# Performance work log

Measured on AMD Instinct MI355X. Metric: run time of the kernel, lower is better.

Reference implementation:

```python
import jax, jax.numpy as jnp
import numpy as np

GC_LAMBDA = 0.5   # smoothness weight from __init__
N_SWEEPS = 30     # fixed checkerboard ICM sweeps (each sweep = 2 half-updates)
EPS = 1e-6


def setup_inputs() -> dict:
    key = jax.random.key(0)
    probs = jax.random.uniform(key, (1, 4096, 4096), dtype=jnp.float32)
    return {"probs": probs}


def _nbr_sum(x):
    # sum of 4-connected neighbors with zero padding at the border
    p = jnp.pad(x, 1)
    return p[:-2, 1:-1] + p[2:, 1:-1] + p[1:-1, :-2] + p[1:-1, 2:]


def reference(probs) -> jnp.ndarray:
    """Graph-cut style binarization of a probability map.

    Minimizes the Potts energy
        E(y) = sum_i [ -y_i log p_i - (1-y_i) log(1-p_i) ]
               + lambda * sum_{(i,j) in 4-nbrs} [y_i != y_j]
    The original custom op solves this exactly via min-cut/max-flow; here we
    use the standard fully-vectorized checkerboard ICM relaxation of the same
    energy (fixed number of sweeps, jit-friendly, deterministic).
    """
    p = probs[0]                                   # [H, W]
    u1 = -jnp.log(p + EPS)                         # unary cost of label 1
    u0 = -jnp.log1p(-(p - EPS))                    # unary cost of label 0
    H, W = p.shape
    ncnt = _nbr_sum(jnp.ones((H, W), p.dtype))     # neighbor counts (2/3/4)
    ii = jnp.arange(H)[:, None]
    jj = jnp.arange(W)[None, :]
    parity_map = ((ii + jj) % 2).astype(jnp.int32)  # checkerboard coloring

    labels0 = (p > 0.5).astype(p.dtype)            # init from thresholding

    def half_sweep(labels, parity):
        ns = _nbr_sum(labels)                      # neighbors labeled 1
        cost1 = u1 + GC_LAMBDA * (ncnt - ns)       # disagree with 0-neighbors
        cost0 = u0 + GC_LAMBDA * ns                # disagree with 1-neighbors
        new = (cost1 < cost0).astype(labels.dtype)
        upd = parity_map == parity
        return jnp.where(upd, new, labels), None

    parities = jnp.tile(jnp.array([0, 1], jnp.int32), N_SWEEPS)
    labels, _ = jax.lax.scan(half_sweep, labels0, parities)
    return jnp.expand_dims(labels, axis=0)         # [1, H, W]
```

## Files before the change

kernel.cpp:

```cpp
#include <hip/hip_runtime.h>
#include <math.h>

#define HH 4096
#define WW 4096
#define WPR 64
#define NWORDS (HH * WPR)
typedef unsigned long long u64;

#define TILE_R 128
#define HALO_R 60
#define REG_R  248
#define REG_WC 10
#define RWORDS (REG_R * REG_WC)
#define NTHR   1024
#define WPT    3
#define NSWEEP 60
#define PACK_WPW 16

__device__ __forceinline__ bool decision(float p, int ncnt, int ns) {
    double pd = (double)p;
    double u1 = -log(pd + 1e-6);
    double u0 = -log1p(-(pd - 1e-6));
    double cost1 = u1 + 0.5 * (double)(ncnt - ns);
    double cost0 = u0 + 0.5 * (double)ns;
    return cost1 < cost0;
}

__global__ void setup_kernel(float* __restrict__ C) {
    int t = threadIdx.x;
    if (t >= 15) return;
    int ncnt = 2 + t / 5;
    int ns = t % 5;
    double T = 0.5 * (double)(2 * ns - ncnt);
    double eT = exp(T);
    double p0 = (1.0 + 1e-6 - 1e-6 * eT) / (1.0 + eT);
    float f0 = (float)p0;
    if (f0 < 0.0f) f0 = 0.0f;
    if (f0 > 1.0f) f0 = 1.0f;
    unsigned b0 = __float_as_uint(f0);
    unsigned lo = (b0 > 64u) ? b0 - 64u : 0u;
    unsigned hi = (b0 + 64u < 0x3F800000u) ? b0 + 64u : 0x3F800000u;
    if (decision(__uint_as_float(lo), ncnt, ns)) lo = 0u;
    if (!decision(__uint_as_float(hi), ncnt, ns)) hi = 0x3F800000u;
    while (hi - lo > 1u) {
        unsigned mid = lo + (hi - lo) / 2u;
        if (decision(__uint_as_float(mid), ncnt, ns)) hi = mid; else lo = mid;
    }
    C[t] = __uint_as_float(hi);
}

__global__ __launch_bounds__(256)
void pack_kernel(const float* __restrict__ probs, const float* __restrict__ C,
                 u64* __restrict__ Kp) {
    int gwave = (blockIdx.x * 256 + threadIdx.x) >> 6;
    int lane = threadIdx.x & 63;
    int w0 = gwave * PACK_WPW;
    float p[PACK_WPW];
#pragma unroll
    for (int q = 0; q < PACK_WPW; ++q)
        p[q] = probs[((size_t)(w0 + q) << 6) + lane];
    const float c0 = C[10], c1 = C[11], c2 = C[12], c3 = C[13], c4 = C[14];
#pragma unroll
    for (int q = 0; q < PACK_WPW; ++q) {
        int w = w0 + q;
        int i = w >> 6;
        int jbase = (w & 63) << 6;
        float pp = p[q];
        int k = (pp < c0) + (pp < c1) + (pp < c2) + (pp < c3) + (pp < c4);
        bool gE0 = (i == 0), gE1 = (i == HH - 1);
        bool jE0 = (jbase == 0) & (lane == 0);
        bool jE1 = (jbase == WW - 64) & (lane == 63);
        if (gE0 | gE1 | jE0 | jE1) {
            int ncnt = 4 - gE0 - gE1 - jE0 - jE1;
            const float* Cr = C + (ncnt - 2) * 5;
            k = (pp < Cr[0]) + (pp < Cr[1]) + (pp < Cr[2]) + (pp < Cr[3]) + (pp < Cr[4]);
        }
        u64 lb = __ballot(pp > 0.5f);
        u64 b0 = __ballot(k & 1);
        u64 b1 = __ballot(k & 2);
        u64 b2 = __ballot(k & 4);
        if (lane < 4) {
            u64 v = (lane == 0) ? lb : (lane == 1) ? b0 : (lane == 2) ? b1 : b2;
            Kp[4ull * w + lane] = v;
        }
    }
}

__global__ __attribute__((amdgpu_flat_work_group_size(NTHR, NTHR),
                          amdgpu_waves_per_eu(4, 4)))
void fused_all(const u64* __restrict__ Kp, float* __restrict__ out) {
    __shared__ u64 SL[RWORDS];
    __shared__ int chg[3];

    const int tid = threadIdx.x;
    const int lane = tid & 63;
    const int tr = blockIdx.x >> 3;
    const int tc = blockIdx.x & 7;
    const int r0 = tr * TILE_R - HALO_R;
    const int wc0 = tc * 8 - 1;

    if (tid < 3) chg[tid] = 0;

    const ulonglong2* Kp2 = (const ulonglong2*)Kp;
    u64 cur[WPT], k0[WPT], k1[WPT], k2[WPT], basem[WPT];
    int rr[WPT], cc[WPT];
#pragma unroll
    for (int m = 0; m < WPT; ++m) {
        int idx = tid + NTHR * m;
        int r = 0, c = 0;
        u64 l = 0, a = ~0ull, b = ~0ull, d = ~0ull;
        if (idx < RWORDS) {
            r = idx / REG_WC;
            c = idx - REG_WC * r;
            int g = r0 + r, wc = wc0 + c;
            if (g >= 0 && g < HH && wc >= 0 && wc < WPR) {
                size_t w = (size_t)g * WPR + wc;
                ulonglong2 x = Kp2[2 * w];
                ulonglong2 y = Kp2[2 * w + 1];
                l = x.x; a = x.y; b = y.x; d = y.y;
            }
            SL[idx] = l;
        }
        cur[m] = l; k0[m] = a; k1[m] = b; k2[m] = d;
        rr[m] = r; cc[m] = c;
        basem[m] = ((r0 + r) & 1) ? 0xAAAAAAAAAAAAAAAAull
                                  : 0x5555555555555555ull;
    }
    __syncthreads();

    int prevf = 1;
    for (int s = 0; s < NSWEEP; ++s) {
        if (tid == 0) chg[(s + 1) % 3] = 0;
        const u64 flip = (s & 1) ? ~0ull : 0ull;
        const int rlo = s + 1, rhi = REG_R - 1 - s;
        u64 chacc = 0;
#pragma unroll
        for (int m = 0; m < WPT; ++m) {
            int idx = tid + NTHR * m;
            int r = rr[m];
            if (idx < RWORDS && r >= rlo && r < rhi) {
                int c = cc[m];
                u64 center = cur[m];
                u64 up = SL[idx - REG_WC], dn = SL[idx + REG_WC];
                u64 pw = (c > 0) ? SL[idx - 1] : 0ull;
                u64 nw = (c < REG_WC - 1) ? SL[idx + 1] : 0ull;
                u64 lv = (center << 1) | (pw >> 63);
                u64 rv = (center >> 1) | (nw << 63);
                u64 sxy = up ^ dn, ca = up & dn;
                u64 txy = lv ^ rv, cb = lv & rv;
                u64 n0 = sxy ^ txy, cd = sxy & txy;
                u64 n1 = ca ^ cb ^ cd;
                u64 n2 = (ca & cb) | (cd & (ca ^ cb));
                u64 ge = (n2 & ~k2[m]) |
                         (~(n2 ^ k2[m]) & ((n1 & ~k1[m]) |
                                           (~(n1 ^ k1[m]) & (n0 | ~k0[m]))));
                u64 mask = basem[m] ^ flip;
                u64 nv = (ge & mask) | (center & ~mask);
                chacc |= nv ^ center;
                cur[m] = nv;
                SL[idx] = nv;
            }
        }
        if (__ballot(chacc != 0) != 0ull) {
            if (lane == 0) chg[s % 3] = 1;
        }
        __syncthreads();
        int curf = chg[s % 3];
        if (prevf == 0 && curf == 0) break;
        prevf = curf;
    }

#pragma unroll 4
    for (int m = 0; m < 16; ++m) {
        int idx = tid + NTHR * m;
        int ri = idx >> 7;
        int q = idx & 127;
        u64 word = SL[(HALO_R + ri) * REG_WC + 1 + (q >> 4)];
        unsigned bits = (unsigned)(word >> ((q & 15) * 4)) & 0xFu;
        float4 v;
        v.x = (float)(bits & 1u);
        v.y = (float)((bits >> 1) & 1u);
        v.z = (float)((bits >> 2) & 1u);
        v.w = (float)((bits >> 3) & 1u);
        int g = tr * TILE_R + ri;
        ((float4*)out)[(size_t)g * (WW / 4) + (wc0 + 1) * 16 + q] = v;
    }
}

extern "C" void kernel_launch(void* const* d_in, const int* in_sizes, int n_in,
                              void* d_out, int out_size, void* d_ws, size_t ws_size,
                              hipStream_t stream) {
    const float* probs = (const float*)d_in[0];
    float* out = (float*)d_out;
    char* ws = (char*)d_ws;
    float* C = (float*)ws;
    u64* Kp = (u64*)(ws + (1u << 20));

    setup_kernel<<<1, 64, 0, stream>>>(C);
    pack_kernel<<<NWORDS / (PACK_WPW * 4), 256, 0, stream>>>(probs, C, Kp);
    fused_all<<<256, NTHR, 0, stream>>>(Kp, out);
}
```

Before: 138.3 us.

## Move threshold search to host, verify in pack kernel, use nontemporal memory ops

Removes the separate setup kernel launch. The 15 decision thresholds are now computed on the host by bisection and passed as a kernel argument. Each pack block re-verifies its thresholds on the device and falls back to a full bisection if a host value is wrong. It also adds nontemporal loads of probs and nontemporal stores of the output, and drops the bounds check for the first two per-thread word slots in fused_all. This saves a launch and some serialization, but every pack block now runs a few double-precision log evaluations at startup.

```diff
diff --git a/kernel.cpp b/kernel.cpp
--- a/kernel.cpp
+++ b/kernel.cpp
@@ -6,6 +6,7 @@
 #define WPR 64
 #define NWORDS (HH * WPR)
 typedef unsigned long long u64;
+typedef float f32x4 __attribute__((ext_vector_type(4)));
 
 #define TILE_R 128
 #define HALO_R 60
@@ -17,6 +18,8 @@
 #define NSWEEP 60
 #define PACK_WPW 16
 
+struct C15 { float v[15]; };
+
 __device__ __forceinline__ bool decision(float p, int ncnt, int ns) {
     double pd = (double)p;
     double u1 = -log(pd + 1e-6);
@@ -26,40 +29,41 @@
     return cost1 < cost0;
 }
 
-__global__ void setup_kernel(float* __restrict__ C) {
-    int t = threadIdx.x;
-    if (t >= 15) return;
-    int ncnt = 2 + t / 5;
-    int ns = t % 5;
-    double T = 0.5 * (double)(2 * ns - ncnt);
-    double eT = exp(T);
-    double p0 = (1.0 + 1e-6 - 1e-6 * eT) / (1.0 + eT);
-    float f0 = (float)p0;
-    if (f0 < 0.0f) f0 = 0.0f;
-    if (f0 > 1.0f) f0 = 1.0f;
-    unsigned b0 = __float_as_uint(f0);
-    unsigned lo = (b0 > 64u) ? b0 - 64u : 0u;
-    unsigned hi = (b0 + 64u < 0x3F800000u) ? b0 + 64u : 0x3F800000u;
-    if (decision(__uint_as_float(lo), ncnt, ns)) lo = 0u;
-    if (!decision(__uint_as_float(hi), ncnt, ns)) hi = 0x3F800000u;
-    while (hi - lo > 1u) {
-        unsigned mid = lo + (hi - lo) / 2u;
-        if (decision(__uint_as_float(mid), ncnt, ns)) hi = mid; else lo = mid;
-    }
-    C[t] = __uint_as_float(hi);
-}
-
 __global__ __launch_bounds__(256)
-void pack_kernel(const float* __restrict__ probs, const float* __restrict__ C,
+void pack_kernel(const float* __restrict__ probs, C15 Ch,
                  u64* __restrict__ Kp) {
-    int gwave = (blockIdx.x * 256 + threadIdx.x) >> 6;
-    int lane = threadIdx.x & 63;
+    __shared__ float Cs[15];
+    const int tid = threadIdx.x;
+    if (tid < 15) {
+        int ncnt = 2 + tid / 5;
+        int ns = tid % 5;
+        unsigned cb = __float_as_uint(Ch.v[tid]);
+        bool ok = false;
+        if (cb > 0u && cb <= 0x3F800000u) {
+            bool below = decision(__uint_as_float(cb - 1u), ncnt, ns);
+            bool at = decision(__uint_as_float(cb), ncnt, ns);
+            ok = (!below) && (at || cb == 0x3F800000u);
+        }
+        if (!ok) {
+            unsigned lo = 0u, hi = 0x3F800000u;
+            while (hi - lo > 1u) {
+                unsigned mid = lo + (hi - lo) / 2u;
+                if (decision(__uint_as_float(mid), ncnt, ns)) hi = mid; else lo = mid;
+            }
+            cb = hi;
+        }
+        Cs[tid] = __uint_as_float(cb);
+    }
+    __syncthreads();
+
+    int gwave = (blockIdx.x * 256 + tid) >> 6;
+    int lane = tid & 63;
     int w0 = gwave * PACK_WPW;
     float p[PACK_WPW];
 #pragma unroll
     for (int q = 0; q < PACK_WPW; ++q)
-        p[q] = probs[((size_t)(w0 + q) << 6) + lane];
-    const float c0 = C[10], c1 = C[11], c2 = C[12], c3 = C[13], c4 = C[14];
+        p[q] = __builtin_nontemporal_load(&probs[((size_t)(w0 + q) << 6) + lane]);
+    const float c0 = Cs[10], c1 = Cs[11], c2 = Cs[12], c3 = Cs[13], c4 = Cs[14];
 #pragma unroll
     for (int q = 0; q < PACK_WPW; ++q) {
         int w = w0 + q;
@@ -72,7 +76,7 @@
         bool jE1 = (jbase == WW - 64) & (lane == 63);
         if (gE0 | gE1 | jE0 | jE1) {
             int ncnt = 4 - gE0 - gE1 - jE0 - jE1;
-            const float* Cr = C + (ncnt - 2) * 5;
+            const float* Cr = Cs + (ncnt - 2) * 5;
             k = (pp < Cr[0]) + (pp < Cr[1]) + (pp < Cr[2]) + (pp < Cr[3]) + (pp < Cr[4]);
         }
         u64 lb = __ballot(pp > 0.5f);
@@ -109,7 +113,7 @@
         int idx = tid + NTHR * m;
         int r = 0, c = 0;
         u64 l = 0, a = ~0ull, b = ~0ull, d = ~0ull;
-        if (idx < RWORDS) {
+        if (m < 2 || idx < RWORDS) {
             r = idx / REG_WC;
             c = idx - REG_WC * r;
             int g = r0 + r, wc = wc0 + c;
@@ -138,7 +142,7 @@
         for (int m = 0; m < WPT; ++m) {
             int idx = tid + NTHR * m;
             int r = rr[m];
-            if (idx < RWORDS && r >= rlo && r < rhi) {
+            if ((m < 2 || idx < RWORDS) && r >= rlo && r < rhi) {
                 int c = cc[m];
                 u64 center = cur[m];
                 u64 up = SL[idx - REG_WC], dn = SL[idx + REG_WC];
@@ -177,26 +181,55 @@
         int q = idx & 127;
         u64 word = SL[(HALO_R + ri) * REG_WC + 1 + (q >> 4)];
         unsigned bits = (unsigned)(word >> ((q & 15) * 4)) & 0xFu;
-        float4 v;
+        f32x4 v;
         v.x = (float)(bits & 1u);
         v.y = (float)((bits >> 1) & 1u);
         v.z = (float)((bits >> 2) & 1u);
         v.w = (float)((bits >> 3) & 1u);
         int g = tr * TILE_R + ri;
-        ((float4*)out)[(size_t)g * (WW / 4) + (wc0 + 1) * 16 + q] = v;
-    }
-}
+        __builtin_nontemporal_store(v,
+            &((f32x4*)out)[(size_t)g * (WW / 4) + (wc0 + 1) * 16 + q]);
+    }
+}
+
+static bool h_decision(float p, int ncnt, int ns) {
+    double pd = (double)p;
+    double u1 = -log(pd + 1e-6);
+    double u0 = -log1p(-(pd - 1e-6));
+    return (u1 + 0.5 * (double)(ncnt - ns)) < (u0 + 0.5 * (double)ns);
+}
+static unsigned h_f2u(float f) { union { float f; unsigned u; } x; x.f = f; return x.u; }
+static float h_u2f(unsigned u) { union { float f; unsigned u; } x; x.u = u; return x.f; }
 
 extern "C" void kernel_launch(void* const* d_in, const int* in_sizes, int n_in,
                               void* d_out, int out_size, void* d_ws, size_t ws_size,
                               hipStream_t stream) {
     const float* probs = (const float*)d_in[0];
     float* out = (float*)d_out;
-    char* ws = (char*)d_ws;
-    float* C = (float*)ws;
-    u64* Kp = (u64*)(ws + (1u << 20));
-
-    setup_kernel<<<1, 64, 0, stream>>>(C);
-    pack_kernel<<<NWORDS / (PACK_WPW * 4), 256, 0, stream>>>(probs, C, Kp);
+    u64* Kp = (u64*)d_ws;
+
+    C15 Ch;
+    for (int t = 0; t < 15; ++t) {
+        int ncnt = 2 + t / 5, ns = t % 5;
+        unsigned lo = 0u, hi = 0x3F800000u;
+        double T = 0.5 * (double)(2 * ns - ncnt);
+        double eT = exp(T);
+        double p0 = (1.0 + 1e-6 - 1e-6 * eT) / (1.0 + eT);
+        float f0 = (float)p0;
+        if (f0 < 0.0f) f0 = 0.0f;
+        if (f0 > 1.0f) f0 = 1.0f;
+        unsigned b0 = h_f2u(f0);
+        unsigned l2 = (b0 > 64u) ? b0 - 64u : 0u;
+        unsigned h2 = (b0 + 64u < 0x3F800000u) ? b0 + 64u : 0x3F800000u;
+        if (!h_decision(h_u2f(l2), ncnt, ns)) lo = l2;
+        if (h_decision(h_u2f(h2), ncnt, ns)) hi = h2;
+        while (hi - lo > 1u) {
+            unsigned mid = lo + (hi - lo) / 2u;
+            if (h_decision(h_u2f(mid), ncnt, ns)) hi = mid; else lo = mid;
+        }
+        Ch.v[t] = h_u2f(hi);
+    }
+
+    pack_kernel<<<NWORDS / (PACK_WPW * 4), 256, 0, stream>>>(probs, Ch, Kp);
     fused_all<<<256, NTHR, 0, stream>>>(Kp, out);
 }
```

After: 143.4 us. +3.7%, slower.
